# Kernel tuning notes

Measured on AMD Instinct MI355X. Metric: run time of the kernel, lower is better.

Reference implementation:

```python
import jax, jax.numpy as jnp
import numpy as np

INPUT_SIZE = 128
HIDDEN_SIZE = 128
OUTPUT_SIZE = 67  # hardcoded in the original module
SEQ_LEN = 512
BATCH = 2048


def setup_inputs() -> dict:
    key = jax.random.key(0)
    ks = jax.random.split(key, 7)
    x = jax.random.normal(ks[0], (INPUT_SIZE, SEQ_LEN, BATCH), dtype=jnp.float32)
    hidden = jax.random.normal(ks[1], (HIDDEN_SIZE, BATCH), dtype=jnp.float32)
    # bernoulli(0.5) mask applied column-wise to the initial hidden state
    drop_mask = jax.random.bernoulli(ks[2], 0.5, (HIDDEN_SIZE, BATCH)).astype(jnp.float32)
    # small init scale so tanh does not saturate
    Wi2h = jax.random.normal(ks[3], (HIDDEN_SIZE, INPUT_SIZE + HIDDEN_SIZE), dtype=jnp.float32) * 0.05
    bi2h = jax.random.normal(ks[4], (HIDDEN_SIZE,), dtype=jnp.float32) * 0.05
    Wi2o = jax.random.normal(ks[5], (OUTPUT_SIZE, HIDDEN_SIZE), dtype=jnp.float32) * 0.05
    bi2o = jax.random.normal(ks[6], (OUTPUT_SIZE,), dtype=jnp.float32) * 0.05
    return {"x": x, "hidden": hidden, "drop_mask": drop_mask,
            "Wi2h": Wi2h, "bi2h": bi2h, "Wi2o": Wi2o, "bi2o": bi2o}


def reference(x, hidden, drop_mask, Wi2h, bi2h, Wi2o, bi2o):
    # x: [input_size, seq_len, batch]; hidden: [hidden_size, batch]
    h0 = hidden * drop_mask  # per-column bernoulli dropout on initial state
    xs = jnp.transpose(x, (1, 0, 2))  # [seq, input_size, batch]

    def step(h, x_t):
        # combined = cat([x_t, h], dim=0).T -> [batch, input+hidden]
        combined = jnp.concatenate([x_t, h], axis=0).T
        h_new = jnp.tanh(combined @ Wi2h.T + bi2h)        # [batch, hidden]
        out = jax.nn.relu(h_new @ Wi2o.T + bi2o)          # [batch, output]
        return h_new.T, out.T                             # carry [hidden, batch], y [output, batch]

    _, ys = jax.lax.scan(step, h0, xs)  # ys: [seq, output, batch]
    Y = jnp.transpose(ys, (1, 0, 2))    # [output, seq, batch]
    return Y
```

## Files before the change

kernel.cpp:

```cpp
#include <hip/hip_runtime.h>
#include <hip/hip_bf16.h>
#include <stdint.h>

#define IN_SZ 128
#define HID 128
#define OUT_SZ 67
#define SEQ 512
#define BATCH 2048
#define BT 8
#define NTHR 768
#define SB (SEQ * BATCH)

typedef __attribute__((ext_vector_type(4))) float f32x4;
typedef __attribute__((ext_vector_type(8))) short s16x8;
typedef __attribute__((ext_vector_type(8))) __bf16 bf16x8;

static __device__ __forceinline__ unsigned short f2bf(float f) {
  union { float f; uint32_t u; } c; c.f = f;
  uint32_t u = c.u;
  uint32_t r = u + 0x7FFFu + ((u >> 16) & 1u);
  return (unsigned short)(r >> 16);
}
static __device__ __forceinline__ uint32_t pk2bf(float lo, float hi) {
  __hip_bfloat162 h2 = __float22bfloat162_rn(float2{lo, hi});
  union { __hip_bfloat162 h; uint32_t u; } c; c.h = h2;
  return c.u;
}
static __device__ __forceinline__ float fast_tanh(float x) {
  float e = __builtin_amdgcn_exp2f(x * 2.885390081777927f);
  float r = __builtin_amdgcn_rcpf(e + 1.f);
  return __builtin_fmaf(-2.f, r, 1.f);
}
static __device__ __forceinline__ void mfma16(f32x4& c, s16x8 a, s16x8 b) {
  c = __builtin_amdgcn_mfma_f32_16x16x32_bf16(
        __builtin_bit_cast(bf16x8, a), __builtin_bit_cast(bf16x8, b), c, 0, 0, 0);
}
#define KOFF(g, j) (4 * (g) + ((j) & 3) + (((j) >> 2) << 4))

static __device__ __forceinline__ void frag_barrier() {
  __builtin_amdgcn_sched_barrier(0);
  asm volatile("s_waitcnt lgkmcnt(0)");
  __builtin_amdgcn_s_barrier();
  __builtin_amdgcn_sched_barrier(0);
}

__global__ __launch_bounds__(NTHR, 1) void rnn_kernel(
    const float* __restrict__ x, const float* __restrict__ hidden,
    const float* __restrict__ mask, const float* __restrict__ Wi2h,
    const float* __restrict__ bi2h, const float* __restrict__ Wi2o,
    const float* __restrict__ bi2o, float* __restrict__ Y) {

  __shared__ s16x8 sX[3][4][64];
  __shared__ s16x8 sH[2][4][64];

  const int tid = threadIdx.x;
  const int wave = tid >> 6;
  const int lane = tid & 63;
  const int g = lane >> 4;
  const int n16 = lane & 15;
  const int bid = ((blockIdx.x & 7) << 5) | (blockIdx.x >> 3);
  const int b0 = bid * BT;

  if (wave < 8) {
    s16x8 W[8];
#pragma unroll
    for (int kt = 0; kt < 8; ++kt) {
      const float* wr = Wi2h + (size_t)(16 * wave + n16) * (IN_SZ + HID);
      s16x8 w8;
#pragma unroll
      for (int j = 0; j < 8; ++j)
        w8[j] = (short)f2bf(wr[32 * kt + KOFF(g, j)]);
      W[kt] = w8;
    }
    f32x4 bhv;
#pragma unroll
    for (int r = 0; r < 4; ++r) bhv[r] = bi2h[16 * wave + 4 * g + r];

    frag_barrier();

    uint32_t* const hdst0 = (uint32_t*)&sH[0][wave >> 1][lane] + (wave & 1) * 2;
    uint32_t* const hdst1 = (uint32_t*)&sH[1][wave >> 1][lane] + (wave & 1) * 2;

#define CSTEP(K)                                                                \
  {                                                                             \
    const int P = (K) & 1;                                                      \
    const int S = (K) % 3;                                                      \
    s16x8 H0 = sH[P][0][lane], H1 = sH[P][1][lane];                             \
    s16x8 H2 = sH[P][2][lane], H3 = sH[P][3][lane];                             \
    s16x8 X0 = sX[S][0][lane], X1 = sX[S][1][lane];                             \
    s16x8 X2 = sX[S][2][lane], X3 = sX[S][3][lane];                             \
    f32x4 a = bhv, a2 = {0.f, 0.f, 0.f, 0.f};                                   \
    f32x4 ax = {0.f, 0.f, 0.f, 0.f}, ax2 = {0.f, 0.f, 0.f, 0.f};                \
    mfma16(a, W[4], H0);   mfma16(a2, W[5], H1);                                \
    mfma16(ax, W[0], X0);  mfma16(ax2, W[1], X1);                               \
    mfma16(a, W[6], H2);   mfma16(a2, W[7], H3);                                \
    mfma16(ax, W[2], X2);  mfma16(ax2, W[3], X3);                               \
    {                                                                           \
      f32x4 s0 = (a + a2) + (ax + ax2);                                         \
      uint32_t hp[2];                                                           \
      hp[0] = pk2bf(fast_tanh(s0[0]), fast_tanh(s0[1]));                        \
      hp[1] = pk2bf(fast_tanh(s0[2]), fast_tanh(s0[3]));                        \
      *(uint64_t*)(P ? hdst0 : hdst1) = *(uint64_t*)hp;                         \
    }                                                                           \
    frag_barrier();                                                             \
  }

    for (int t6 = 0; t6 < 510; t6 += 6) {
      CSTEP(0) CSTEP(1) CSTEP(2) CSTEP(3) CSTEP(4) CSTEP(5)
    }
    CSTEP(0) CSTEP(1)
#undef CSTEP

  } else {
    const int sv = wave - 8;
    const int svl = (sv << 6) | lane;

    const int ntile = (sv < 2) ? 2 : (sv == 2 ? 1 : 0);
    const int tk0 = 2 * sv;
    s16x8 wO[2][4];
    f32x4 bov[2];
    uint32_t ybase[2];
#pragma unroll
    for (int ot = 0; ot < 2; ++ot) {
      const int tk = tk0 + ot;
      const bool tv = (ot < ntile);
#pragma unroll
      for (int kk = 0; kk < 4; ++kk) {
        s16x8 a;
#pragma unroll
        for (int j = 0; j < 8; ++j) {
          int m = 16 * tk + n16;
          a[j] = (short)((tv && m < OUT_SZ)
                         ? f2bf(Wi2o[(size_t)m * HID + 32 * kk + KOFF(g, j)]) : 0);
        }
        wO[ot][kk] = a;
      }
#pragma unroll
      for (int r = 0; r < 4; ++r) {
        int m = 16 * tk + 4 * g + r;
        bov[ot][r] = (tv && m < OUT_SZ) ? bi2o[m] : 0.f;
      }
      ybase[ot] = (uint32_t)(16 * tk + 4 * g) * (uint32_t)SB + (uint32_t)(b0 + n16);
    }

    int skkA, sqA, slaneA, skkB, sqB, slaneB;
    uint32_t xaA0, xaA1, xaB0, xaB1;
    {
      int d = 2 * svl;
      int rp = d >> 3, lc = d & 7, R0 = 2 * rp;
      int r5 = R0 & 31;
      int sg = (r5 < 16) ? (r5 >> 2) : ((r5 - 16) >> 2);
      skkA = R0 >> 5;
      sqA = ((r5 & 2) >> 1) + ((r5 < 16) ? 0 : 2);
      slaneA = (sg << 4) | lc;
      xaA0 = ((uint32_t)R0 * (uint32_t)SB + (uint32_t)(b0 + lc)) * 4u;
      xaA1 = ((uint32_t)(R0 + 1) * (uint32_t)SB + (uint32_t)(b0 + lc)) * 4u;
      d = 2 * svl + 1;
      rp = d >> 3; lc = d & 7; R0 = 2 * rp;
      r5 = R0 & 31;
      sg = (r5 < 16) ? (r5 >> 2) : ((r5 - 16) >> 2);
      skkB = R0 >> 5;
      sqB = ((r5 & 2) >> 1) + ((r5 < 16) ? 0 : 2);
      slaneB = (sg << 4) | lc;
      xaB0 = ((uint32_t)R0 * (uint32_t)SB + (uint32_t)(b0 + lc)) * 4u;
      xaB1 = ((uint32_t)(R0 + 1) * (uint32_t)SB + (uint32_t)(b0 + lc)) * 4u;
    }
    const char* const xB = (const char*)x;

#pragma unroll
    for (int tt = 0; tt < 2; ++tt) {
      const uint32_t to = (uint32_t)tt * (BATCH * 4u);
      float a0 = *(const float*)(xB + xaA0 + to);
      float a1 = *(const float*)(xB + xaA1 + to);
      float c0 = *(const float*)(xB + xaB0 + to);
      float c1 = *(const float*)(xB + xaB1 + to);
      ((uint32_t*)&sX[tt][skkA][slaneA])[sqA] = pk2bf(a0, a1);
      ((uint32_t*)&sX[tt][skkB][slaneB])[sqB] = pk2bf(c0, c1);
    }
    {
      const uint32_t hA0 = (xaA0 / (4u * SB)) * (uint32_t)BATCH + (uint32_t)(b0 + ((2 * svl) & 7));
      const uint32_t hA1 = (xaA1 / (4u * SB)) * (uint32_t)BATCH + (uint32_t)(b0 + ((2 * svl) & 7));
      const uint32_t hB0 = (xaB0 / (4u * SB)) * (uint32_t)BATCH + (uint32_t)(b0 + ((2 * svl + 1) & 7));
      const uint32_t hB1 = (xaB1 / (4u * SB)) * (uint32_t)BATCH + (uint32_t)(b0 + ((2 * svl + 1) & 7));
      float a0 = hidden[(size_t)hA0] * mask[(size_t)hA0];
      float a1 = hidden[(size_t)hA1] * mask[(size_t)hA1];
      float c0 = hidden[(size_t)hB0] * mask[(size_t)hB0];
      float c1 = hidden[(size_t)hB1] * mask[(size_t)hB1];
      ((uint32_t*)&sH[0][skkA][slaneA])[sqA] = pk2bf(a0, a1);
      ((uint32_t*)&sH[0][skkB][slaneB])[sqB] = pk2bf(c0, c1);
    }
    float q0[4], q1[4], q2[4], q3[4], q4[4], q5[4];
#define FILLQ(Q, T)                                                             \
    {                                                                           \
      const uint32_t to = (uint32_t)(T) * (BATCH * 4u);                         \
      Q[0] = *(const float*)(xB + xaA0 + to);                                   \
      Q[1] = *(const float*)(xB + xaA1 + to);                                   \
      Q[2] = *(const float*)(xB + xaB0 + to);                                   \
      Q[3] = *(const float*)(xB + xaB1 + to);                                   \
    }
    FILLQ(q0, 2) FILLQ(q1, 3) FILLQ(q2, 4) FILLQ(q3, 5) FILLQ(q4, 6) FILLQ(q5, 7)
    frag_barrier();

#define SSTEP(K, Q)                                                             \
  {                                                                             \
    const int t = t6 + (K);                                                     \
    const int SW = ((K) + 2) % 3;                                               \
    ((uint32_t*)&sX[SW][skkA][slaneA])[sqA] = pk2bf(Q[0], Q[1]);                \
    ((uint32_t*)&sX[SW][skkB][slaneB])[sqB] = pk2bf(Q[2], Q[3]);                \
    {                                                                           \
      const int tn = (t + 8 > 511) ? 511 : t + 8;                               \
      FILLQ(Q, tn)                                                              \
    }                                                                           \
    if (ntile > 0 && t > 0) {                                                   \
      const int P = (K) & 1;                                                    \
      s16x8 H0 = sH[P][0][lane], H1 = sH[P][1][lane];                           \
      s16x8 H2 = sH[P][2][lane], H3 = sH[P][3][lane];                           \
      const uint32_t ty = (uint32_t)(t - 1) * (uint32_t)BATCH;                  \
      _Pragma("unroll")                                                         \
      for (int ot = 0; ot < 2; ++ot) {                                          \
        if (ot < ntile) {                                                       \
          const int tk = tk0 + ot;                                              \
          f32x4 ao = bov[ot];                                                   \
          mfma16(ao, wO[ot][0], H0); mfma16(ao, wO[ot][1], H1);                 \
          mfma16(ao, wO[ot][2], H2); mfma16(ao, wO[ot][3], H3);                 \
          if (n16 < BT) {                                                       \
            _Pragma("unroll")                                                   \
            for (int r = 0; r < 4; ++r)                                         \
              if (16 * tk + 4 * g + r < OUT_SZ)                                 \
                Y[(size_t)(ybase[ot] + (uint32_t)r * SB + ty)] = fmaxf(ao[r], 0.f); \
          }                                                                     \
        }                                                                       \
      }                                                                         \
    }                                                                           \
    frag_barrier();                                                             \
  }

    for (int t6 = 0; t6 < 510; t6 += 6) {
      SSTEP(0, q0) SSTEP(1, q1) SSTEP(2, q2) SSTEP(3, q3) SSTEP(4, q4) SSTEP(5, q5)
    }
    {
      const int t6 = 510;
      SSTEP(0, q0) SSTEP(1, q1)
    }
#undef SSTEP
#undef FILLQ

    if (ntile > 0) {
      s16x8 H0 = sH[0][0][lane], H1 = sH[0][1][lane];
      s16x8 H2 = sH[0][2][lane], H3 = sH[0][3][lane];
      const uint32_t ty = 511u * (uint32_t)BATCH;
#pragma unroll
      for (int ot = 0; ot < 2; ++ot) {
        if (ot < ntile) {
          const int tk = tk0 + ot;
          f32x4 ao = bov[ot];
          mfma16(ao, wO[ot][0], H0); mfma16(ao, wO[ot][1], H1);
          mfma16(ao, wO[ot][2], H2); mfma16(ao, wO[ot][3], H3);
          if (n16 < BT) {
#pragma unroll
            for (int r = 0; r < 4; ++r)
              if (16 * tk + 4 * g + r < OUT_SZ)
                Y[(size_t)(ybase[ot] + (uint32_t)r * SB + ty)] = fmaxf(ao[r], 0.f);
          }
        }
      }
    }
  }
}

extern "C" void kernel_launch(void* const* d_in, const int* in_sizes, int n_in,
                              void* d_out, int out_size, void* d_ws, size_t ws_size,
                              hipStream_t stream) {
  const float* x      = (const float*)d_in[0];
  const float* hidden = (const float*)d_in[1];
  const float* mask   = (const float*)d_in[2];
  const float* Wi2h   = (const float*)d_in[3];
  const float* bi2h   = (const float*)d_in[4];
  const float* Wi2o   = (const float*)d_in[5];
  const float* bi2o   = (const float*)d_in[6];
  float* Y = (float*)d_out;
  (void)in_sizes; (void)n_in; (void)out_size; (void)d_ws; (void)ws_size;
  rnn_kernel<<<dim3(BATCH / BT), dim3(NTHR), 0, stream>>>(
      x, hidden, mask, Wi2h, bi2h, Wi2o, bi2o, Y);
}
```

Baseline: 482.6 us.

## Halve block to 384 threads, merging output projection into compute waves

The block drops from 12 waves to 6. Four compute waves now each produce two 16-row hidden tiles instead of one, and they also run the output projection and Y stores themselves. Two loader waves stream x into shared memory, four columns per lane. This cuts barrier participants and removes the separate output waves. In exchange, each compute wave does about twice the MFMA work per step on the serial recurrence path, plus the output MFMAs.

```diff
diff --git a/kernel.cpp b/kernel.cpp
--- a/kernel.cpp
+++ b/kernel.cpp
@@ -8,7 +8,7 @@
 #define SEQ 512
 #define BATCH 2048
 #define BT 8
-#define NTHR 768
+#define NTHR 384
 #define SB (SEQ * BATCH)
 
 typedef __attribute__((ext_vector_type(4))) float f32x4;
@@ -61,69 +61,36 @@
   const int bid = ((blockIdx.x & 7) << 5) | (blockIdx.x >> 3);
   const int b0 = bid * BT;
 
-  if (wave < 8) {
-    s16x8 W[8];
+  if (wave < 4) {
+    s16x8 W0[8], W1[8];
 #pragma unroll
     for (int kt = 0; kt < 8; ++kt) {
-      const float* wr = Wi2h + (size_t)(16 * wave + n16) * (IN_SZ + HID);
-      s16x8 w8;
-#pragma unroll
-      for (int j = 0; j < 8; ++j)
-        w8[j] = (short)f2bf(wr[32 * kt + KOFF(g, j)]);
-      W[kt] = w8;
-    }
-    f32x4 bhv;
-#pragma unroll
-    for (int r = 0; r < 4; ++r) bhv[r] = bi2h[16 * wave + 4 * g + r];
-
-    frag_barrier();
-
-    uint32_t* const hdst0 = (uint32_t*)&sH[0][wave >> 1][lane] + (wave & 1) * 2;
-    uint32_t* const hdst1 = (uint32_t*)&sH[1][wave >> 1][lane] + (wave & 1) * 2;
-
-#define CSTEP(K)                                                                \
-  {                                                                             \
-    const int P = (K) & 1;                                                      \
-    const int S = (K) % 3;                                                      \
-    s16x8 H0 = sH[P][0][lane], H1 = sH[P][1][lane];                             \
-    s16x8 H2 = sH[P][2][lane], H3 = sH[P][3][lane];                             \
-    s16x8 X0 = sX[S][0][lane], X1 = sX[S][1][lane];                             \
-    s16x8 X2 = sX[S][2][lane], X3 = sX[S][3][lane];                             \
-    f32x4 a = bhv, a2 = {0.f, 0.f, 0.f, 0.f};                                   \
-    f32x4 ax = {0.f, 0.f, 0.f, 0.f}, ax2 = {0.f, 0.f, 0.f, 0.f};                \
-    mfma16(a, W[4], H0);   mfma16(a2, W[5], H1);                                \
-    mfma16(ax, W[0], X0);  mfma16(ax2, W[1], X1);                               \
-    mfma16(a, W[6], H2);   mfma16(a2, W[7], H3);                                \
-    mfma16(ax, W[2], X2);  mfma16(ax2, W[3], X3);                               \
-    {                                                                           \
-      f32x4 s0 = (a + a2) + (ax + ax2);                                         \
-      uint32_t hp[2];                                                           \
-      hp[0] = pk2bf(fast_tanh(s0[0]), fast_tanh(s0[1]));                        \
-      hp[1] = pk2bf(fast_tanh(s0[2]), fast_tanh(s0[3]));                        \
-      *(uint64_t*)(P ? hdst0 : hdst1) = *(uint64_t*)hp;                         \
-    }                                                                           \
-    frag_barrier();                                                             \
-  }
-
-    for (int t6 = 0; t6 < 510; t6 += 6) {
-      CSTEP(0) CSTEP(1) CSTEP(2) CSTEP(3) CSTEP(4) CSTEP(5)
-    }
-    CSTEP(0) CSTEP(1)
-#undef CSTEP
-
-  } else {
-    const int sv = wave - 8;
-    const int svl = (sv << 6) | lane;
-
-    const int ntile = (sv < 2) ? 2 : (sv == 2 ? 1 : 0);
-    const int tk0 = 2 * sv;
+      const float* wr0 = Wi2h + (size_t)(16 * (2 * wave + 0) + n16) * (IN_SZ + HID);
+      const float* wr1 = Wi2h + (size_t)(16 * (2 * wave + 1) + n16) * (IN_SZ + HID);
+      s16x8 w8a, w8b;
+#pragma unroll
+      for (int j = 0; j < 8; ++j) {
+        w8a[j] = (short)f2bf(wr0[32 * kt + KOFF(g, j)]);
+        w8b[j] = (short)f2bf(wr1[32 * kt + KOFF(g, j)]);
+      }
+      W0[kt] = w8a; W1[kt] = w8b;
+    }
+    f32x4 bhv0, bhv1;
+#pragma unroll
+    for (int r = 0; r < 4; ++r) {
+      bhv0[r] = bi2h[16 * (2 * wave + 0) + 4 * g + r];
+      bhv1[r] = bi2h[16 * (2 * wave + 1) + 4 * g + r];
+    }
+
+    const int nt = (wave == 3) ? 2 : 1;
     s16x8 wO[2][4];
     f32x4 bov[2];
     uint32_t ybase[2];
+    int trow[2];
 #pragma unroll
     for (int ot = 0; ot < 2; ++ot) {
-      const int tk = tk0 + ot;
-      const bool tv = (ot < ntile);
+      const int tk = (ot == 0) ? wave : 4;
+      const bool tv = (ot < ((wave == 3) ? 2 : 1));
 #pragma unroll
       for (int kk = 0; kk < 4; ++kk) {
         s16x8 a;
@@ -141,92 +108,66 @@
         bov[ot][r] = (tv && m < OUT_SZ) ? bi2o[m] : 0.f;
       }
       ybase[ot] = (uint32_t)(16 * tk + 4 * g) * (uint32_t)SB + (uint32_t)(b0 + n16);
-    }
-
-    int skkA, sqA, slaneA, skkB, sqB, slaneB;
-    uint32_t xaA0, xaA1, xaB0, xaB1;
-    {
-      int d = 2 * svl;
-      int rp = d >> 3, lc = d & 7, R0 = 2 * rp;
-      int r5 = R0 & 31;
-      int sg = (r5 < 16) ? (r5 >> 2) : ((r5 - 16) >> 2);
-      skkA = R0 >> 5;
-      sqA = ((r5 & 2) >> 1) + ((r5 < 16) ? 0 : 2);
-      slaneA = (sg << 4) | lc;
-      xaA0 = ((uint32_t)R0 * (uint32_t)SB + (uint32_t)(b0 + lc)) * 4u;
-      xaA1 = ((uint32_t)(R0 + 1) * (uint32_t)SB + (uint32_t)(b0 + lc)) * 4u;
-      d = 2 * svl + 1;
-      rp = d >> 3; lc = d & 7; R0 = 2 * rp;
-      r5 = R0 & 31;
-      sg = (r5 < 16) ? (r5 >> 2) : ((r5 - 16) >> 2);
-      skkB = R0 >> 5;
-      sqB = ((r5 & 2) >> 1) + ((r5 < 16) ? 0 : 2);
-      slaneB = (sg << 4) | lc;
-      xaB0 = ((uint32_t)R0 * (uint32_t)SB + (uint32_t)(b0 + lc)) * 4u;
-      xaB1 = ((uint32_t)(R0 + 1) * (uint32_t)SB + (uint32_t)(b0 + lc)) * 4u;
-    }
-    const char* const xB = (const char*)x;
-
-#pragma unroll
-    for (int tt = 0; tt < 2; ++tt) {
-      const uint32_t to = (uint32_t)tt * (BATCH * 4u);
-      float a0 = *(const float*)(xB + xaA0 + to);
-      float a1 = *(const float*)(xB + xaA1 + to);
-      float c0 = *(const float*)(xB + xaB0 + to);
-      float c1 = *(const float*)(xB + xaB1 + to);
-      ((uint32_t*)&sX[tt][skkA][slaneA])[sqA] = pk2bf(a0, a1);
-      ((uint32_t*)&sX[tt][skkB][slaneB])[sqB] = pk2bf(c0, c1);
-    }
-    {
-      const uint32_t hA0 = (xaA0 / (4u * SB)) * (uint32_t)BATCH + (uint32_t)(b0 + ((2 * svl) & 7));
-      const uint32_t hA1 = (xaA1 / (4u * SB)) * (uint32_t)BATCH + (uint32_t)(b0 + ((2 * svl) & 7));
-      const uint32_t hB0 = (xaB0 / (4u * SB)) * (uint32_t)BATCH + (uint32_t)(b0 + ((2 * svl + 1) & 7));
-      const uint32_t hB1 = (xaB1 / (4u * SB)) * (uint32_t)BATCH + (uint32_t)(b0 + ((2 * svl + 1) & 7));
-      float a0 = hidden[(size_t)hA0] * mask[(size_t)hA0];
-      float a1 = hidden[(size_t)hA1] * mask[(size_t)hA1];
-      float c0 = hidden[(size_t)hB0] * mask[(size_t)hB0];
-      float c1 = hidden[(size_t)hB1] * mask[(size_t)hB1];
-      ((uint32_t*)&sH[0][skkA][slaneA])[sqA] = pk2bf(a0, a1);
-      ((uint32_t*)&sH[0][skkB][slaneB])[sqB] = pk2bf(c0, c1);
-    }
-    float q0[4], q1[4], q2[4], q3[4], q4[4], q5[4];
-#define FILLQ(Q, T)                                                             \
-    {                                                                           \
-      const uint32_t to = (uint32_t)(T) * (BATCH * 4u);                         \
-      Q[0] = *(const float*)(xB + xaA0 + to);                                   \
-      Q[1] = *(const float*)(xB + xaA1 + to);                                   \
-      Q[2] = *(const float*)(xB + xaB0 + to);                                   \
-      Q[3] = *(const float*)(xB + xaB1 + to);                                   \
-    }
-    FILLQ(q0, 2) FILLQ(q1, 3) FILLQ(q2, 4) FILLQ(q3, 5) FILLQ(q4, 6) FILLQ(q5, 7)
+      trow[ot] = 16 * tk + 4 * g;
+    }
+
+    {
+      const int cc = (b0 + n16 < BATCH) ? (b0 + n16) : (BATCH - 1);
+      union { s16x8 v; uint32_t d[4]; } u;
+#pragma unroll
+      for (int q = 0; q < 4; ++q) {
+        int r0 = 32 * wave + KOFF(g, 2 * q);
+        int r1 = 32 * wave + KOFF(g, 2 * q + 1);
+        float h0 = hidden[(size_t)r0 * BATCH + cc] * mask[(size_t)r0 * BATCH + cc];
+        float h1 = hidden[(size_t)r1 * BATCH + cc] * mask[(size_t)r1 * BATCH + cc];
+        u.d[q] = pk2bf(h0, h1);
+      }
+      sH[0][wave][lane] = u.v;
+    }
     frag_barrier();
 
-#define SSTEP(K, Q)                                                             \
+#define CSTEP(K)                                                                \
   {                                                                             \
     const int t = t6 + (K);                                                     \
-    const int SW = ((K) + 2) % 3;                                               \
-    ((uint32_t*)&sX[SW][skkA][slaneA])[sqA] = pk2bf(Q[0], Q[1]);                \
-    ((uint32_t*)&sX[SW][skkB][slaneB])[sqB] = pk2bf(Q[2], Q[3]);                \
+    const int P = (K) & 1;                                                      \
+    const int S = (K) % 3;                                                      \
+    s16x8 X0 = sX[S][0][lane], X1 = sX[S][1][lane];                             \
+    s16x8 X2 = sX[S][2][lane], X3 = sX[S][3][lane];                             \
+    s16x8 H0 = sH[P][0][lane], H1 = sH[P][1][lane];                             \
+    s16x8 H2 = sH[P][2][lane], H3 = sH[P][3][lane];                             \
+    f32x4 a = bhv0, a2 = {0.f, 0.f, 0.f, 0.f};                                  \
+    f32x4 b = bhv1, b2 = {0.f, 0.f, 0.f, 0.f};                                  \
+    mfma16(a, W0[0], X0);  mfma16(a2, W0[1], X1);                               \
+    mfma16(b, W1[0], X0);  mfma16(b2, W1[1], X1);                               \
+    mfma16(a, W0[2], X2);  mfma16(a2, W0[3], X3);                               \
+    mfma16(b, W1[2], X2);  mfma16(b2, W1[3], X3);                               \
+    mfma16(a, W0[4], H0);  mfma16(a2, W0[5], H1);                               \
+    mfma16(b, W1[4], H0);  mfma16(b2, W1[5], H1);                               \
+    mfma16(a, W0[6], H2);  mfma16(a2, W0[7], H3);                               \
+    mfma16(b, W1[6], H2);  mfma16(b2, W1[7], H3);                               \
+             \
     {                                                                           \
-      const int tn = (t + 8 > 511) ? 511 : t + 8;                               \
-      FILLQ(Q, tn)                                                              \
-    }                                                                           \
-    if (ntile > 0 && t > 0) {                                                   \
-      const int P = (K) & 1;                                                    \
-      s16x8 H0 = sH[P][0][lane], H1 = sH[P][1][lane];                           \
-      s16x8 H2 = sH[P][2][lane], H3 = sH[P][3][lane];                           \
+      f32x4 s0 = a + a2, s1 = b + b2;                                           \
+      union { s16x8 v; uint32_t d[4]; } u;                                      \
+      u.d[0] = pk2bf(fast_tanh(s0[0]), fast_tanh(s0[1]));                       \
+      u.d[1] = pk2bf(fast_tanh(s0[2]), fast_tanh(s0[3]));                       \
+      u.d[2] = pk2bf(fast_tanh(s1[0]), fast_tanh(s1[1]));                       \
+      u.d[3] = pk2bf(fast_tanh(s1[2]), fast_tanh(s1[3]));                       \
+      sH[P ^ 1][wave][lane] = u.v;                                              \
+    }                                                                           \
+      \
+    if (t > 0) {                                                                \
       const uint32_t ty = (uint32_t)(t - 1) * (uint32_t)BATCH;                  \
       _Pragma("unroll")                                                         \
       for (int ot = 0; ot < 2; ++ot) {                                          \
-        if (ot < ntile) {                                                       \
-          const int tk = tk0 + ot;                                              \
+        if (ot < nt) {                                                          \
           f32x4 ao = bov[ot];                                                   \
           mfma16(ao, wO[ot][0], H0); mfma16(ao, wO[ot][1], H1);                 \
           mfma16(ao, wO[ot][2], H2); mfma16(ao, wO[ot][3], H3);                 \
           if (n16 < BT) {                                                       \
             _Pragma("unroll")                                                   \
             for (int r = 0; r < 4; ++r)                                         \
-              if (16 * tk + 4 * g + r < OUT_SZ)                                 \
+              if (trow[ot] + r < OUT_SZ)                                        \
                 Y[(size_t)(ybase[ot] + (uint32_t)r * SB + ty)] = fmaxf(ao[r], 0.f); \
           }                                                                     \
         }                                                                       \
@@ -236,35 +177,97 @@
   }
 
     for (int t6 = 0; t6 < 510; t6 += 6) {
-      SSTEP(0, q0) SSTEP(1, q1) SSTEP(2, q2) SSTEP(3, q3) SSTEP(4, q4) SSTEP(5, q5)
+      CSTEP(0) CSTEP(1) CSTEP(2) CSTEP(3) CSTEP(4) CSTEP(5)
     }
     {
       const int t6 = 510;
-      SSTEP(0, q0) SSTEP(1, q1)
-    }
-#undef SSTEP
-#undef FILLQ
-
-    if (ntile > 0) {
+      CSTEP(0) CSTEP(1)
+    }
+#undef CSTEP
+
+    {
       s16x8 H0 = sH[0][0][lane], H1 = sH[0][1][lane];
       s16x8 H2 = sH[0][2][lane], H3 = sH[0][3][lane];
       const uint32_t ty = 511u * (uint32_t)BATCH;
 #pragma unroll
       for (int ot = 0; ot < 2; ++ot) {
-        if (ot < ntile) {
-          const int tk = tk0 + ot;
+        if (ot < nt) {
           f32x4 ao = bov[ot];
           mfma16(ao, wO[ot][0], H0); mfma16(ao, wO[ot][1], H1);
           mfma16(ao, wO[ot][2], H2); mfma16(ao, wO[ot][3], H3);
           if (n16 < BT) {
 #pragma unroll
             for (int r = 0; r < 4; ++r)
-              if (16 * tk + 4 * g + r < OUT_SZ)
+              if (trow[ot] + r < OUT_SZ)
                 Y[(size_t)(ybase[ot] + (uint32_t)r * SB + ty)] = fmaxf(ao[r], 0.f);
           }
         }
       }
     }
+
+  } else {
+    const int svl = ((wave - 4) << 6) | lane;
+    const int rp = svl >> 1;
+    const int R0 = 2 * rp;
+    const int lcb = (svl & 1) * 4;
+    const int skk = R0 >> 5;
+    const int r5 = R0 & 31;
+    const int sg = (r5 < 16) ? (r5 >> 2) : ((r5 - 16) >> 2);
+    const int sq = ((r5 & 2) >> 1) + ((r5 < 16) ? 0 : 2);
+    const int slb = sg << 4;
+    const char* const xB = (const char*)x;
+    const uint32_t xr0 = ((uint32_t)R0 * (uint32_t)SB + (uint32_t)b0) * 4u;
+    const uint32_t xr1 = ((uint32_t)(R0 + 1) * (uint32_t)SB + (uint32_t)b0) * 4u;
+
+#pragma unroll
+    for (int tt = 0; tt < 2; ++tt) {
+      const uint32_t to = (uint32_t)tt * (BATCH * 4u);
+#pragma unroll
+      for (int i = 0; i < 4; ++i) {
+        const int lc = lcb + i;
+        float v0 = *(const float*)(xB + xr0 + to + 4u * lc);
+        float v1 = *(const float*)(xB + xr1 + to + 4u * lc);
+        ((uint32_t*)&sX[tt][skk][slb | lc])[sq] = pk2bf(v0, v1);
+      }
+    }
+    float q0[8], q1[8], q2[8], q3[8], q4[8], q5[8];
+#define FILLQ(Q, T)                                                             \
+    {                                                                           \
+      const uint32_t to = (uint32_t)(T) * (BATCH * 4u);                         \
+      _Pragma("unroll")                                                         \
+      for (int i = 0; i < 4; ++i) {                                             \
+        Q[2 * i]     = *(const float*)(xB + xr0 + to + 4u * (lcb + i));         \
+        Q[2 * i + 1] = *(const float*)(xB + xr1 + to + 4u * (lcb + i));         \
+      }                                                                         \
+    }
+    FILLQ(q0, 2) FILLQ(q1, 3) FILLQ(q2, 4) FILLQ(q3, 5) FILLQ(q4, 6) FILLQ(q5, 7)
+    frag_barrier();
+
+#define SSTEP(K, Q)                                                             \
+  {                                                                             \
+    const int t = t6 + (K);                                                     \
+    const int SW = ((K) + 2) % 3;                                               \
+    _Pragma("unroll")                                                           \
+    for (int i = 0; i < 4; ++i) {                                               \
+      const int lc = lcb + i;                                                   \
+      ((uint32_t*)&sX[SW][skk][slb | lc])[sq] = pk2bf(Q[2 * i], Q[2 * i + 1]);  \
+    }                                                                           \
+    {                                                                           \
+      const int tn = (t + 8 > 511) ? 511 : t + 8;                               \
+      FILLQ(Q, tn)                                                              \
+    }                                                                           \
+    frag_barrier();                                                             \
+  }
+
+    for (int t6 = 0; t6 < 510; t6 += 6) {
+      SSTEP(0, q0) SSTEP(1, q1) SSTEP(2, q2) SSTEP(3, q3) SSTEP(4, q4) SSTEP(5, q5)
+    }
+    {
+      const int t6 = 510;
+      SSTEP(0, q0) SSTEP(1, q1)
+    }
+#undef SSTEP
+#undef FILLQ
   }
 }
 
```

Measured after the change: 434.3 us (median of 2 runs). 10.0% less time.
